# Performance work log

Hardware: AMD Instinct MI355X
Metric: run time of the kernel (lower is better)

Reference implementation:

```python
import jax, jax.numpy as jnp
import numpy as np

SURROGATE_ALPHA = 2.0  # ATan surrogate sharpness (spikingjelly-style default)

@jax.custom_vjp
def spike_fn(x):
    return jnp.where(x > 0, 1.0, 0.0)

def _spike_fwd(x):
    return spike_fn(x), x

def _spike_bwd(x, g):
    # ATan surrogate gradient: alpha/2 / (1 + (pi/2 * alpha * x)^2)
    sg = SURROGATE_ALPHA / 2.0 / (1.0 + (jnp.pi / 2.0 * SURROGATE_ALPHA * x) ** 2)
    return (g * sg,)

spike_fn.defvjp(_spike_fwd, _spike_bwd)

def setup_inputs() -> dict:
    key = jax.random.key(0)
    B, N, T, D = 4, 1024, 128, 128  # [batch, nodes, time, feat]
    x = jax.random.normal(key, (B, N, T, D), dtype=jnp.float32)
    decay = jnp.zeros((D,), jnp.float32)  # nn.initializers.constant(0.0)
    v_th = jnp.zeros((D,), jnp.float32)   # nn.initializers.constant(0.0)
    return {"x": x, "decay": decay, "v_th": v_th}

def reference(x, decay, v_th):
    # time axis is dim 2 in the original module
    x_seq = jnp.moveaxis(x, 2, 0)  # [T, B, N, D]
    d = jax.nn.sigmoid(decay)          # per-feature learnable decay in (0,1)
    th = jax.nn.sigmoid(v_th) + 0.1    # per-feature learnable threshold > 0.1

    def scan_fn(v, x_t):
        v = v * d + x_t                        # leaky integrate
        s = spike_fn(v - th)                   # fire
        v = v * (1.0 - jax.lax.stop_gradient(s))  # hard reset (detached)
        return v, s

    v_init = jnp.zeros_like(x_seq[0])
    _, spikes = jax.lax.scan(scan_fn, v_init, x_seq)
    return jnp.moveaxis(spikes, 0, 2)  # back to [B, N, T, D]
```

## Files before the change

### kernel.cpp

```cpp
#include <hip/hip_runtime.h>
#include <math.h>


#define T_STEPS 128
#define D_FEAT  128
#define GROUPS  (D_FEAT / 4)

__global__ __launch_bounds__(256)
void plif_fwd_kernel(const float4* __restrict__ x,
                     const float*  __restrict__ decay,
                     const float*  __restrict__ vth,
                     float4* __restrict__ out)
{
    const int tid = blockIdx.x * blockDim.x + threadIdx.x;
    const int g   = tid & (GROUPS - 1);
    const int row = tid >> 5;

    const size_t base = (size_t)row * (size_t)T_STEPS * GROUPS + (size_t)g;
    const float4* __restrict__ xr = x + base;
    float4* __restrict__       orw = out + base;

    const int d0 = g * 4;
    float dec0 = 1.0f / (1.0f + expf(-decay[d0 + 0]));
    float dec1 = 1.0f / (1.0f + expf(-decay[d0 + 1]));
    float dec2 = 1.0f / (1.0f + expf(-decay[d0 + 2]));
    float dec3 = 1.0f / (1.0f + expf(-decay[d0 + 3]));
    float th0  = 1.0f / (1.0f + expf(-vth[d0 + 0])) + 0.1f;
    float th1  = 1.0f / (1.0f + expf(-vth[d0 + 1])) + 0.1f;
    float th2  = 1.0f / (1.0f + expf(-vth[d0 + 2])) + 0.1f;
    float th3  = 1.0f / (1.0f + expf(-vth[d0 + 3])) + 0.1f;

    float v0 = 0.0f, v1 = 0.0f, v2 = 0.0f, v3 = 0.0f;

#pragma unroll 4
    for (int t = 0; t < T_STEPS; ++t) {
        const float4 xv = xr[(size_t)t * GROUPS];

        v0 = __fadd_rn(__fmul_rn(v0, dec0), xv.x);
        const float s0 = (__fsub_rn(v0, th0) > 0.0f) ? 1.0f : 0.0f;
        v0 = (s0 != 0.0f) ? 0.0f : v0;
        v1 = __fadd_rn(__fmul_rn(v1, dec1), xv.y);
        const float s1 = (__fsub_rn(v1, th1) > 0.0f) ? 1.0f : 0.0f;
        v1 = (s1 != 0.0f) ? 0.0f : v1;
        v2 = __fadd_rn(__fmul_rn(v2, dec2), xv.z);
        const float s2 = (__fsub_rn(v2, th2) > 0.0f) ? 1.0f : 0.0f;
        v2 = (s2 != 0.0f) ? 0.0f : v2;
        v3 = __fadd_rn(__fmul_rn(v3, dec3), xv.w);
        const float s3 = (__fsub_rn(v3, th3) > 0.0f) ? 1.0f : 0.0f;
        v3 = (s3 != 0.0f) ? 0.0f : v3;

        orw[(size_t)t * GROUPS] = make_float4(s0, s1, s2, s3);
    }
}

extern "C" void kernel_launch(void* const* d_in, const int* in_sizes, int n_in,
                              void* d_out, int out_size, void* d_ws, size_t ws_size,
                              hipStream_t stream)
{
    const float* x     = (const float*)d_in[0];
    const float* decay = (const float*)d_in[1];
    const float* vth   = (const float*)d_in[2];
    float*       out   = (float*)d_out;

    const int total   = in_sizes[0];
    const int rows    = total / (T_STEPS * D_FEAT);
    const int threads = rows * GROUPS;
    const int block   = 256;

    plif_fwd_kernel<<<threads / block, block, 0, stream>>>(
        (const float4*)x, decay, vth, (float4*)out);
}
```

Baseline: 111.4 us.

## Use float2 per thread, nontemporal loads/stores, and direct threshold compare

Each thread now handles two features instead of four, which doubles the thread count to raise memory-level parallelism across the 128-step sequential scan. Loads and stores use nontemporal builtins so streaming data bypasses cache retention. The spike test compares v > th directly instead of subtracting first, and the unroll factor rises to 8. Narrower 8-byte accesses may use fewer bytes per memory instruction than the previous float4 accesses.

```diff
diff --git a/kernel.cpp b/kernel.cpp
--- a/kernel.cpp
+++ b/kernel.cpp
@@ -4,52 +4,49 @@
 
 #define T_STEPS 128
 #define D_FEAT  128
-#define GROUPS  (D_FEAT / 4)
+#define GROUPS  (D_FEAT / 2)
+
+typedef float f32x2 __attribute__((ext_vector_type(2)));
 
 __global__ __launch_bounds__(256)
-void plif_fwd_kernel(const float4* __restrict__ x,
-                     const float*  __restrict__ decay,
-                     const float*  __restrict__ vth,
-                     float4* __restrict__ out)
+void plif_fwd_kernel(const f32x2* __restrict__ x,
+                     const float* __restrict__ decay,
+                     const float* __restrict__ vth,
+                     f32x2* __restrict__ out)
 {
     const int tid = blockIdx.x * blockDim.x + threadIdx.x;
     const int g   = tid & (GROUPS - 1);
-    const int row = tid >> 5;
+    const int row = tid >> 6;
 
     const size_t base = (size_t)row * (size_t)T_STEPS * GROUPS + (size_t)g;
-    const float4* __restrict__ xr = x + base;
-    float4* __restrict__       orw = out + base;
+    const f32x2* __restrict__ xr  = x + base;
+    f32x2* __restrict__       orw = out + base;
 
-    const int d0 = g * 4;
-    float dec0 = 1.0f / (1.0f + expf(-decay[d0 + 0]));
-    float dec1 = 1.0f / (1.0f + expf(-decay[d0 + 1]));
-    float dec2 = 1.0f / (1.0f + expf(-decay[d0 + 2]));
-    float dec3 = 1.0f / (1.0f + expf(-decay[d0 + 3]));
-    float th0  = 1.0f / (1.0f + expf(-vth[d0 + 0])) + 0.1f;
-    float th1  = 1.0f / (1.0f + expf(-vth[d0 + 1])) + 0.1f;
-    float th2  = 1.0f / (1.0f + expf(-vth[d0 + 2])) + 0.1f;
-    float th3  = 1.0f / (1.0f + expf(-vth[d0 + 3])) + 0.1f;
+    const int d0 = g * 2;
+    const float dec0 = 1.0f / (1.0f + expf(-decay[d0 + 0]));
+    const float dec1 = 1.0f / (1.0f + expf(-decay[d0 + 1]));
+    const float th0  = 1.0f / (1.0f + expf(-vth[d0 + 0])) + 0.1f;
+    const float th1  = 1.0f / (1.0f + expf(-vth[d0 + 1])) + 0.1f;
 
-    float v0 = 0.0f, v1 = 0.0f, v2 = 0.0f, v3 = 0.0f;
+    float v0 = 0.0f, v1 = 0.0f;
 
-#pragma unroll 4
+#pragma unroll 8
     for (int t = 0; t < T_STEPS; ++t) {
-        const float4 xv = xr[(size_t)t * GROUPS];
+        const f32x2 xv = __builtin_nontemporal_load(xr + (size_t)t * GROUPS);
 
         v0 = __fadd_rn(__fmul_rn(v0, dec0), xv.x);
-        const float s0 = (__fsub_rn(v0, th0) > 0.0f) ? 1.0f : 0.0f;
-        v0 = (s0 != 0.0f) ? 0.0f : v0;
+        const bool f0 = (v0 > th0);
+        const float s0 = f0 ? 1.0f : 0.0f;
+        v0 = f0 ? 0.0f : v0;
         v1 = __fadd_rn(__fmul_rn(v1, dec1), xv.y);
-        const float s1 = (__fsub_rn(v1, th1) > 0.0f) ? 1.0f : 0.0f;
-        v1 = (s1 != 0.0f) ? 0.0f : v1;
-        v2 = __fadd_rn(__fmul_rn(v2, dec2), xv.z);
-        const float s2 = (__fsub_rn(v2, th2) > 0.0f) ? 1.0f : 0.0f;
-        v2 = (s2 != 0.0f) ? 0.0f : v2;
-        v3 = __fadd_rn(__fmul_rn(v3, dec3), xv.w);
-        const float s3 = (__fsub_rn(v3, th3) > 0.0f) ? 1.0f : 0.0f;
-        v3 = (s3 != 0.0f) ? 0.0f : v3;
+        const bool f1 = (v1 > th1);
+        const float s1 = f1 ? 1.0f : 0.0f;
+        v1 = f1 ? 0.0f : v1;
 
-        orw[(size_t)t * GROUPS] = make_float4(s0, s1, s2, s3);
+        f32x2 sv;
+        sv.x = s0;
+        sv.y = s1;
+        __builtin_nontemporal_store(sv, orw + (size_t)t * GROUPS);
     }
 }
 
@@ -68,5 +65,5 @@
     const int block   = 256;
 
     plif_fwd_kernel<<<threads / block, block, 0, stream>>>(
-        (const float4*)x, decay, vth, (float4*)out);
+        (const f32x2*)x, decay, vth, (f32x2*)out);
 }
```

New measurement: 104.2 us. 6.5% less time.
